# Performance work log

Hardware: AMD Instinct MI355X
Metric: run time of the kernel (lower is better)

Reference implementation:

```python
import jax, jax.numpy as jnp
import numpy as np

N = 100000
E = 1600000
F_IN = 512
HID = 8
HEADS = 8
NCLS = 16
NEG_SLOPE = 0.2
EPS = 1e-16


def gat_conv(x, W, att_src, att_dst, bias, src, dst, heads, ch, concat):
    n = x.shape[0]
    xl = (x @ W).reshape(n, heads, ch)              # [N,H,C]
    a_src = (xl * att_src).sum(-1)                  # [N,H]
    a_dst = (xl * att_dst).sum(-1)                  # [N,H]
    alpha = jax.nn.leaky_relu(a_src[src] + a_dst[dst], NEG_SLOPE)  # [E,H]
    amax = jax.ops.segment_max(alpha, dst, num_segments=n)         # [N,H]
    ex = jnp.exp(alpha - amax[dst])                                 # [E,H]
    denom = jax.ops.segment_sum(ex, dst, num_segments=n)           # [N,H]
    coef = ex / (denom[dst] + EPS)                                  # [E,H]
    msg = xl[src] * coef[:, :, None]                                # [E,H,C]
    out = jax.ops.segment_sum(msg, dst, num_segments=n)            # [N,H,C]
    out = out.reshape(n, heads * ch) if concat else out.mean(axis=1)
    return out + bias


def setup_inputs() -> dict:
    key = jax.random.key(0)
    ks = jax.random.split(key, 12)
    x = jax.random.normal(ks[0], (N, F_IN), dtype=jnp.float32)
    edge_index = jax.random.randint(ks[1], (2, E), 0, N, dtype=jnp.int32)
    s1 = 1.0 / np.sqrt(F_IN)
    s2 = 1.0 / np.sqrt(HID * HEADS)
    return {
        "x": x,
        "edge_index": edge_index,
        "W1": jax.random.normal(ks[2], (F_IN, HEADS * HID), dtype=jnp.float32) * s1,
        "att_src1": jax.random.normal(ks[3], (HEADS, HID), dtype=jnp.float32),
        "att_dst1": jax.random.normal(ks[4], (HEADS, HID), dtype=jnp.float32),
        "bias1": jnp.zeros((HEADS * HID,), dtype=jnp.float32),
        "W2": jax.random.normal(ks[5], (HEADS * HID, NCLS), dtype=jnp.float32) * s2,
        "att_src2": jax.random.normal(ks[6], (1, NCLS), dtype=jnp.float32),
        "att_dst2": jax.random.normal(ks[7], (1, NCLS), dtype=jnp.float32),
        "bias2": jnp.zeros((NCLS,), dtype=jnp.float32),
    }


def reference(x, edge_index, W1, att_src1, att_dst1, bias1, W2, att_src2, att_dst2, bias2):
    src, dst = edge_index[0], edge_index[1]
    # eval mode: all dropout layers are identity
    h = gat_conv(x, W1, att_src1, att_dst1, bias1, src, dst, HEADS, HID, True)
    h = jax.nn.elu(h)
    out = gat_conv(h, W2, att_src2, att_dst2, bias2, src, dst, 1, NCLS, False)
    return out
```

## Files before the change

kernel.cpp:

```cpp
#include <hip/hip_runtime.h>
#include <math.h>

#define N_NODES 100000
#define N_EDGES 1600000
#define F_IN    512
#define HID     8
#define HEADS   8
#define NCLS    16
#define NEG_SLOPE 0.2f
#define EPS_F   1e-16f
#define DEG_CAP 64
#define G1_BLOCKS 782
#define CSR_EPB 1024
#define CSR_BLOCKS 1563

__device__ __forceinline__ float lrelu(float a) {
    return a >= 0.f ? a : NEG_SLOPE * a;
}
__device__ __forceinline__ unsigned short f2bf_rne(float f) {
    unsigned b = __float_as_uint(f);
    b += 0x7FFFu + ((b >> 16) & 1u);
    return (unsigned short)(b >> 16);
}
__device__ __forceinline__ float bf2f(unsigned short u) {
    return __uint_as_float(((unsigned)u) << 16);
}

__global__ __launch_bounds__(256) void fused1_kernel(
    const float* __restrict__ x, const float* __restrict__ W1,
    const float* __restrict__ att_src, const float* __restrict__ att_dst,
    unsigned short* __restrict__ xl1b,
    float* __restrict__ a_src1, float* __restrict__ a_dst1,
    const int* __restrict__ src, const int* __restrict__ dst,
    int* __restrict__ cnt, int* __restrict__ csr_src) {
    __shared__ float xs[128][33];
    __shared__ float wsh[32][68];
    const int tid = threadIdx.x;

    if (blockIdx.x >= G1_BLOCKS) {
        int e0 = (blockIdx.x - G1_BLOCKS) * CSR_EPB + tid;
        int d[4], s[4];
        bool v[4];
#pragma unroll
        for (int q = 0; q < 4; q++) {
            int e = e0 + q * 256;
            v[q] = e < N_EDGES;
            if (v[q]) { d[q] = dst[e]; s[q] = src[e]; }
        }
        int pos[4];
#pragma unroll
        for (int q = 0; q < 4; q++)
            if (v[q]) pos[q] = atomicAdd(&cnt[d[q]], 1);
#pragma unroll
        for (int q = 0; q < 4; q++)
            if (v[q] && pos[q] < DEG_CAP)
                csr_src[(size_t)d[q] * DEG_CAP + pos[q]] = s[q];
        return;
    }

    const int nb  = blockIdx.x * 128;
    const int ng  = tid >> 3;
    const int cg  = tid & 7;

    float acc[4][8];
#pragma unroll
    for (int i = 0; i < 4; i++)
#pragma unroll
        for (int j = 0; j < 8; j++) acc[i][j] = 0.f;

    for (int kb = 0; kb < F_IN; kb += 32) {
#pragma unroll
        for (int q = 0; q < 4; q++) {
            int idx = tid + q * 256;
            int nl  = idx >> 3;
            int kq  = (idx & 7) * 4;
            int node = nb + nl; if (node >= N_NODES) node = N_NODES - 1;
            float4 vv = *(const float4*)&x[(size_t)node * F_IN + kb + kq];
            xs[nl][kq + 0] = vv.x; xs[nl][kq + 1] = vv.y;
            xs[nl][kq + 2] = vv.z; xs[nl][kq + 3] = vv.w;
        }
#pragma unroll
        for (int q = 0; q < 2; q++) {
            int idx = tid + q * 256;
            int kk  = idx >> 4;
            int cq  = (idx & 15) * 4;
            *(float4*)&wsh[kk][cq] = *(const float4*)&W1[(size_t)(kb + kk) * 64 + cq];
        }
        __syncthreads();
#pragma unroll
        for (int kk = 0; kk < 32; kk++) {
            float xa0 = xs[ng * 4 + 0][kk];
            float xa1 = xs[ng * 4 + 1][kk];
            float xa2 = xs[ng * 4 + 2][kk];
            float xa3 = xs[ng * 4 + 3][kk];
            float4 w0 = *(const float4*)&wsh[kk][cg * 8];
            float4 w1 = *(const float4*)&wsh[kk][cg * 8 + 4];
            float wa[8] = {w0.x, w0.y, w0.z, w0.w, w1.x, w1.y, w1.z, w1.w};
#pragma unroll
            for (int j = 0; j < 8; j++) {
                acc[0][j] += xa0 * wa[j];
                acc[1][j] += xa1 * wa[j];
                acc[2][j] += xa2 * wa[j];
                acc[3][j] += xa3 * wa[j];
            }
        }
        __syncthreads();
    }
    float4 s0 = *(const float4*)&att_src[cg * 8];
    float4 s1 = *(const float4*)&att_src[cg * 8 + 4];
    float4 d0 = *(const float4*)&att_dst[cg * 8];
    float4 d1 = *(const float4*)&att_dst[cg * 8 + 4];
    float sv[8] = {s0.x, s0.y, s0.z, s0.w, s1.x, s1.y, s1.z, s1.w};
    float dv[8] = {d0.x, d0.y, d0.z, d0.w, d1.x, d1.y, d1.z, d1.w};
#pragma unroll
    for (int i = 0; i < 4; i++) {
        int node = nb + ng * 4 + i;
        if (node < N_NODES) {
            unsigned pk[4];
#pragma unroll
            for (int j = 0; j < 4; j++)
                pk[j] = (unsigned)f2bf_rne(acc[i][2 * j]) |
                        ((unsigned)f2bf_rne(acc[i][2 * j + 1]) << 16);
            *(uint4*)&xl1b[(size_t)node * 64 + cg * 8] =
                make_uint4(pk[0], pk[1], pk[2], pk[3]);
            float as = 0.f, ad = 0.f;
#pragma unroll
            for (int j = 0; j < 8; j++) { as += acc[i][j] * sv[j]; ad += acc[i][j] * dv[j]; }
            a_src1[node * 8 + cg] = as;
            a_dst1[node * 8 + cg] = ad;
        }
    }
}

__global__ __launch_bounds__(256) void aggr1_kernel(
    const int* __restrict__ cnt, const int* __restrict__ csr_src,
    const float* __restrict__ a_src1, const float* __restrict__ a_dst1,
    const unsigned short* __restrict__ xl1b,
    const float* __restrict__ bias1, const float* __restrict__ W2,
    const float* __restrict__ att_src2, const float* __restrict__ att_dst2,
    float* __restrict__ xl2, float* __restrict__ a_src2, float* __restrict__ a_dst2) {
    __shared__ float w2s[64][17];
    __shared__ float b1s[64];
    __shared__ float hbuf[8][64];
    const int tid  = threadIdx.x;
    const int w    = tid >> 6;
    const int lane = tid & 63;
    const int l32  = lane & 31;
    const int hf   = lane >> 5;
    const int c0   = l32 * 2;
    const int h    = l32 >> 2;

#pragma unroll
    for (int q = 0; q < 4; q++) {
        int idx = tid * 4 + q;
        w2s[idx >> 4][idx & 15] = W2[idx];
    }
    if (tid < 64) b1s[tid] = bias1[tid];
    __syncthreads();

    const int nl = w * 2 + hf;
    const int n  = blockIdx.x * 8 + nl;
    const int* bucket = &csr_src[(size_t)n * DEG_CAP];
    int c = cnt[n]; c = c < DEG_CAP ? c : DEG_CAP;
    int cw = c; { int co = __shfl_xor(c, 32); cw = cw > co ? cw : co; }
    float ad = a_dst1[n * 8 + h];
    float l = 0.f, acc0 = 0.f, acc1 = 0.f;

    for (int i = 0; i < cw; i += 8) {
        int s[8]; float e[8], x0[8], x1[8];
#pragma unroll
        for (int q = 0; q < 8; q++) {
            int ii = i + q; ii = ii < c ? ii : (c > 0 ? c - 1 : 0);
            s[q] = bucket[ii];
        }
#pragma unroll
        for (int q = 0; q < 8; q++) {
            int ss = s[q]; ss = ss < 0 ? 0 : ss;
            s[q] = ss >= N_NODES ? N_NODES - 1 : ss;
        }
#pragma unroll
        for (int q = 0; q < 8; q++) {
            unsigned v = *(const unsigned*)&xl1b[(size_t)s[q] * 64 + c0];
            x0[q] = bf2f((unsigned short)(v & 0xFFFFu));
            x1[q] = bf2f((unsigned short)(v >> 16));
        }
#pragma unroll
        for (int q = 0; q < 8; q++) {
            float al = lrelu(a_src1[s[q] * 8 + h] + ad);
            float ee = __expf(al);
            e[q] = (i + q < c) ? ee : 0.f;
        }
#pragma unroll
        for (int q = 0; q < 8; q++) {
            l += e[q]; acc0 += e[q] * x0[q]; acc1 += e[q] * x1[q];
        }
    }

    float dinv = 1.f / (l + EPS_F);
    float h0 = acc0 * dinv + b1s[c0];
    float h1 = acc1 * dinv + b1s[c0 + 1];
    h0 = h0 > 0.f ? h0 : (__expf(h0) - 1.f);
    h1 = h1 > 0.f ? h1 : (__expf(h1) - 1.f);
    hbuf[nl][c0] = h0; hbuf[nl][c0 + 1] = h1;
    __syncthreads();

    const int j  = l32 & 15;
    const int kh = l32 >> 4;
    float p = 0.f;
#pragma unroll
    for (int k2 = 0; k2 < 32; k2++) {
        int k = kh * 32 + k2;
        p += hbuf[nl][k] * w2s[k][j];
    }
    p += __shfl_xor(p, 16);
    float ss = p * att_src2[j];
    float dd = p * att_dst2[j];
#pragma unroll
    for (int mm = 8; mm >= 1; mm >>= 1) {
        ss += __shfl_xor(ss, mm);
        dd += __shfl_xor(dd, mm);
    }
    if (l32 == 0) { a_src2[n] = ss; a_dst2[n] = dd; }
    if (l32 < 16) xl2[(size_t)n * 16 + l32] = p;
}

__global__ __launch_bounds__(256) void aggr2_kernel(
    const int* __restrict__ cnt, const int* __restrict__ csr_src,
    const float* __restrict__ a_src2, const float* __restrict__ a_dst2,
    const float* __restrict__ xl2, const float* __restrict__ bias2,
    float* __restrict__ out) {
    int idx = blockIdx.x * 256 + threadIdx.x;
    int n = idx >> 4;
    int j = idx & 15;
    if (n >= N_NODES) return;
    const int* bucket = &csr_src[(size_t)n * DEG_CAP];
    int c = cnt[n]; c = c < DEG_CAP ? c : DEG_CAP;
    int cw = c;
    { int co = __shfl_xor(c, 16); cw = cw > co ? cw : co; }
    { int co = __shfl_xor(cw, 32); cw = cw > co ? cw : co; }
    float ad = a_dst2[n];
    float l = 0.f, acc = 0.f;
    for (int i = 0; i < cw; i += 8) {
        int s[8]; float e[8];
#pragma unroll
        for (int q = 0; q < 8; q++) {
            int ii = i + q; ii = ii < c ? ii : (c > 0 ? c - 1 : 0);
            s[q] = bucket[ii];
        }
#pragma unroll
        for (int q = 0; q < 8; q++) {
            int ssx = s[q]; ssx = ssx < 0 ? 0 : ssx;
            s[q] = ssx >= N_NODES ? N_NODES - 1 : ssx;
        }
#pragma unroll
        for (int q = 0; q < 8; q++) {
            float al = lrelu(a_src2[s[q]] + ad);
            float ee = __expf(al);
            e[q] = (i + q < c) ? ee : 0.f;
        }
#pragma unroll
        for (int q = 0; q < 8; q++) {
            float xv = xl2[(size_t)s[q] * 16 + j];
            l += e[q]; acc += e[q] * xv;
        }
    }
    out[(size_t)n * 16 + j] = acc / (l + EPS_F) + bias2[j];
}

extern "C" void kernel_launch(void* const* d_in, const int* in_sizes, int n_in,
                              void* d_out, int out_size, void* d_ws, size_t ws_size,
                              hipStream_t stream) {
    const float* x        = (const float*)d_in[0];
    const int*   ei       = (const int*)d_in[1];
    const float* W1       = (const float*)d_in[2];
    const float* att_src1 = (const float*)d_in[3];
    const float* att_dst1 = (const float*)d_in[4];
    const float* bias1    = (const float*)d_in[5];
    const float* W2       = (const float*)d_in[6];
    const float* att_src2 = (const float*)d_in[7];
    const float* att_dst2 = (const float*)d_in[8];
    const float* bias2    = (const float*)d_in[9];
    float* out = (float*)d_out;

    const int* src = ei;
    const int* dst = ei + N_EDGES;

    float* ws = (float*)d_ws;
    float* a_src1 = ws;
    float* a_dst1 = a_src1 + (size_t)N_NODES * 8;
    float* xl2    = a_dst1 + (size_t)N_NODES * 8;
    float* a_src2 = xl2 + (size_t)N_NODES * 16;
    float* a_dst2 = a_src2 + N_NODES;
    int*   cnt    = (int*)(a_dst2 + N_NODES);
    int*   csr_src= cnt + N_NODES;
    unsigned short* xl1b = (unsigned short*)(csr_src + (size_t)N_NODES * DEG_CAP);

    hipMemsetAsync(cnt, 0, (size_t)N_NODES * sizeof(int), stream);

    fused1_kernel<<<G1_BLOCKS + CSR_BLOCKS, 256, 0, stream>>>(
        x, W1, att_src1, att_dst1, xl1b, a_src1, a_dst1,
        src, dst, cnt, csr_src);

    aggr1_kernel<<<N_NODES / 8, 256, 0, stream>>>(
        cnt, csr_src, a_src1, a_dst1, xl1b, bias1, W2, att_src2, att_dst2,
        xl2, a_src2, a_dst2);

    aggr2_kernel<<<(N_NODES * 16 + 255) / 256, 256, 0, stream>>>(
        cnt, csr_src, a_src2, a_dst2, xl2, bias2, out);
}
```

Baseline: 438.2 us.

## Remap aggr1 to one wavefront per node with edge-parallel lanes

Rewrites the layer-1 aggregation so each 64-lane wavefront handles one node. Eight edge groups of eight lanes each cover one head per lane, and each lane does a 16-byte vector load of eight bf16 features. The bucket indices are loaded once per lane and broadcast with shuffles, and partial sums are combined with an xor-shuffle reduction at the end. This cuts redundant per-head a_src loads and serial per-edge latency, at the cost of extra shuffle reductions and twice as many blocks.

New measurement: 452.5 us. +3.3%, slower.

```diff
diff --git a/kernel.cpp b/kernel.cpp
--- a/kernel.cpp
+++ b/kernel.cpp
@@ -25,6 +25,12 @@
 __device__ __forceinline__ float bf2f(unsigned short u) {
     return __uint_as_float(((unsigned)u) << 16);
 }
+__device__ __forceinline__ float bf_lo(unsigned v) {
+    return __uint_as_float(v << 16);
+}
+__device__ __forceinline__ float bf_hi(unsigned v) {
+    return __uint_as_float(v & 0xFFFF0000u);
+}
 
 __global__ __launch_bounds__(256) void fused1_kernel(
     const float* __restrict__ x, const float* __restrict__ W1,
@@ -140,79 +146,81 @@
     const float* __restrict__ att_src2, const float* __restrict__ att_dst2,
     float* __restrict__ xl2, float* __restrict__ a_src2, float* __restrict__ a_dst2) {
     __shared__ float w2s[64][17];
-    __shared__ float b1s[64];
-    __shared__ float hbuf[8][64];
+    __shared__ float hbuf[4][64];
     const int tid  = threadIdx.x;
     const int w    = tid >> 6;
     const int lane = tid & 63;
-    const int l32  = lane & 31;
-    const int hf   = lane >> 5;
-    const int c0   = l32 * 2;
-    const int h    = l32 >> 2;
+    const int g    = lane & 7;
+    const int e    = lane >> 3;
 
 #pragma unroll
     for (int q = 0; q < 4; q++) {
         int idx = tid * 4 + q;
         w2s[idx >> 4][idx & 15] = W2[idx];
     }
-    if (tid < 64) b1s[tid] = bias1[tid];
     __syncthreads();
 
-    const int nl = w * 2 + hf;
-    const int n  = blockIdx.x * 8 + nl;
-    const int* bucket = &csr_src[(size_t)n * DEG_CAP];
+    const int n = blockIdx.x * 4 + w;
     int c = cnt[n]; c = c < DEG_CAP ? c : DEG_CAP;
-    int cw = c; { int co = __shfl_xor(c, 32); cw = cw > co ? cw : co; }
-    float ad = a_dst1[n * 8 + h];
-    float l = 0.f, acc0 = 0.f, acc1 = 0.f;
-
-    for (int i = 0; i < cw; i += 8) {
-        int s[8]; float e[8], x0[8], x1[8];
-#pragma unroll
-        for (int q = 0; q < 8; q++) {
-            int ii = i + q; ii = ii < c ? ii : (c > 0 ? c - 1 : 0);
-            s[q] = bucket[ii];
-        }
-#pragma unroll
-        for (int q = 0; q < 8; q++) {
-            int ss = s[q]; ss = ss < 0 ? 0 : ss;
-            s[q] = ss >= N_NODES ? N_NODES - 1 : ss;
-        }
-#pragma unroll
-        for (int q = 0; q < 8; q++) {
-            unsigned v = *(const unsigned*)&xl1b[(size_t)s[q] * 64 + c0];
-            x0[q] = bf2f((unsigned short)(v & 0xFFFFu));
-            x1[q] = bf2f((unsigned short)(v >> 16));
-        }
-#pragma unroll
-        for (int q = 0; q < 8; q++) {
-            float al = lrelu(a_src1[s[q] * 8 + h] + ad);
-            float ee = __expf(al);
-            e[q] = (i + q < c) ? ee : 0.f;
-        }
-#pragma unroll
-        for (int q = 0; q < 8; q++) {
-            l += e[q]; acc0 += e[q] * x0[q]; acc1 += e[q] * x1[q];
-        }
+    int b = csr_src[(size_t)n * DEG_CAP + lane];
+    b = b < 0 ? 0 : b;
+    b = b >= N_NODES ? N_NODES - 1 : b;
+    float ad = a_dst1[n * 8 + g];
+
+    float l = 0.f;
+    float acc[8];
+#pragma unroll
+    for (int k = 0; k < 8; k++) acc[k] = 0.f;
+
+    for (int i = 0; i < c; i += 8) {
+        int idx = i + e;
+        int s = __shfl(b, idx);
+        uint4 vv = *(const uint4*)&xl1b[(size_t)s * 64 + g * 8];
+        float as = a_src1[s * 8 + g];
+        float al = lrelu(as + ad);
+        float ee = __expf(al);
+        ee = (idx < c) ? ee : 0.f;
+        l += ee;
+        acc[0] += ee * bf_lo(vv.x);
+        acc[1] += ee * bf_hi(vv.x);
+        acc[2] += ee * bf_lo(vv.y);
+        acc[3] += ee * bf_hi(vv.y);
+        acc[4] += ee * bf_lo(vv.z);
+        acc[5] += ee * bf_hi(vv.z);
+        acc[6] += ee * bf_lo(vv.w);
+        acc[7] += ee * bf_hi(vv.w);
+    }
+
+#pragma unroll
+    for (int mask = 8; mask <= 32; mask <<= 1) {
+        l += __shfl_xor(l, mask);
+#pragma unroll
+        for (int k = 0; k < 8; k++) acc[k] += __shfl_xor(acc[k], mask);
     }
 
     float dinv = 1.f / (l + EPS_F);
-    float h0 = acc0 * dinv + b1s[c0];
-    float h1 = acc1 * dinv + b1s[c0 + 1];
-    h0 = h0 > 0.f ? h0 : (__expf(h0) - 1.f);
-    h1 = h1 > 0.f ? h1 : (__expf(h1) - 1.f);
-    hbuf[nl][c0] = h0; hbuf[nl][c0 + 1] = h1;
+    float hv[8];
+#pragma unroll
+    for (int k = 0; k < 8; k++) {
+        float t = acc[k] * dinv + bias1[g * 8 + k];
+        hv[k] = t > 0.f ? t : (__expf(t) - 1.f);
+    }
+    if (e == 0) {
+        *(float4*)&hbuf[w][g * 8]     = make_float4(hv[0], hv[1], hv[2], hv[3]);
+        *(float4*)&hbuf[w][g * 8 + 4] = make_float4(hv[4], hv[5], hv[6], hv[7]);
+    }
     __syncthreads();
 
-    const int j  = l32 & 15;
-    const int kh = l32 >> 4;
+    const int j  = lane & 15;
+    const int kh = lane >> 4;
     float p = 0.f;
 #pragma unroll
-    for (int k2 = 0; k2 < 32; k2++) {
-        int k = kh * 32 + k2;
-        p += hbuf[nl][k] * w2s[k][j];
+    for (int k2 = 0; k2 < 16; k2++) {
+        int k = kh * 16 + k2;
+        p += hbuf[w][k] * w2s[k][j];
     }
     p += __shfl_xor(p, 16);
+    p += __shfl_xor(p, 32);
     float ss = p * att_src2[j];
     float dd = p * att_dst2[j];
 #pragma unroll
@@ -220,8 +228,8 @@
         ss += __shfl_xor(ss, mm);
         dd += __shfl_xor(dd, mm);
     }
-    if (l32 == 0) { a_src2[n] = ss; a_dst2[n] = dd; }
-    if (l32 < 16) xl2[(size_t)n * 16 + l32] = p;
+    if (lane == 0) { a_src2[n] = ss; a_dst2[n] = dd; }
+    if (lane < 16) xl2[(size_t)n * 16 + lane] = p;
 }
 
 __global__ __launch_bounds__(256) void aggr2_kernel(
@@ -301,7 +309,7 @@
         x, W1, att_src1, att_dst1, xl1b, a_src1, a_dst1,
         src, dst, cnt, csr_src);
 
-    aggr1_kernel<<<N_NODES / 8, 256, 0, stream>>>(
+    aggr1_kernel<<<N_NODES / 4, 256, 0, stream>>>(
         cnt, csr_src, a_src1, a_dst1, xl1b, bias1, W2, att_src2, att_dst2,
         xl2, a_src2, a_dst2);
 
```
